# Kernel optimization log

Hardware: AMD Instinct MI355X
Metric: run time of the kernel (lower is better)

## Reference

```python
import jax, jax.numpy as jnp
import numpy as np

B, C, T, L = 32, 21, 512, 336
FREQ = T // 2 + 1  # 257
EPS = 1e-5


def setup_inputs() -> dict:
    key = jax.random.key(0)
    k1, k2, k3 = jax.random.split(key, 3)
    z = jax.random.normal(k1, (B, C, T), dtype=jnp.float32)
    affine_w = jnp.ones((C,), dtype=jnp.float32)
    affine_b = jnp.zeros((C,), dtype=jnp.float32)
    head_w = jax.random.normal(k2, (L, T * FREQ), dtype=jnp.float32) * 0.002
    head_b = jax.random.normal(k3, (L,), dtype=jnp.float32) * 0.01
    return {"z": z, "affine_w": affine_w, "affine_b": affine_b,
            "head_w": head_w, "head_b": head_b}


def _bases(T, FREQ):
    # t = arange(0,1,1/T); rows p: cos(2*pi*p*t), -sin(2*pi*p*t); DC row scaled by 0.5
    t = jnp.arange(T, dtype=jnp.float32) / T
    p = jnp.arange(FREQ, dtype=jnp.float32)
    ang = 2.0 * jnp.pi * p[:, None] * t[None, :]          # (FREQ, T)
    cosb = jnp.cos(ang).at[0].multiply(0.5)
    sinb = (-jnp.sin(ang)).at[0].multiply(0.5)
    return cosb, sinb


def reference(z, affine_w, affine_b, head_w, head_b):
    # RevIN 'norm' over time axis (unbiased=False variance)
    mean = jnp.mean(z, axis=-1, keepdims=True)              # (B,C,1)
    std = jnp.sqrt(jnp.var(z, axis=-1, keepdims=True) + EPS)
    w = affine_w[None, :, None]
    b = affine_b[None, :, None]
    zn = (z - mean) / std * w + b                           # (B,C,T)

    X = jnp.fft.rfft(zn, axis=-1) / T * 2.0                 # (B,C,FREQ) complex
    cosb, sinb = _bases(T, FREQ)
    # outer-product basis expansion -> (B,C,FREQ,T)
    basis = (jnp.einsum('bcp,pt->bcpt', jnp.real(X), cosb)
             + jnp.einsum('bcp,pt->bcpt', jnp.imag(X), sinb)).astype(jnp.float32)
    flat = basis.reshape(B, C, FREQ * T)                    # (B,C,head_nf)

    out = jnp.einsum('bcn,ln->bcl', flat, head_w) + head_b  # (B,C,L)

    # RevIN 'denorm'
    out = (out - b) / (w + EPS * EPS) * std + mean
    return out
```

## Files before the change

kernel.cpp:

```cpp
#include <hip/hip_runtime.h>
#include <math.h>

#define BB 32
#define CC 21
#define TT 512
#define LL 336
#define FREQ 257
#define NBC (BB*CC)
#define WROW (FREQ*TT)

__device__ __constant__ float kAngStep = 6.28318530717958647692f / 512.0f;

__global__ __launch_bounds__(256) void k0_stats(const float* __restrict__ z,
                                                float* __restrict__ meanv,
                                                float* __restrict__ stdv) {
    int row  = blockIdx.x * 4 + (threadIdx.x >> 6);
    int lane = threadIdx.x & 63;
    const float* zr = z + (size_t)row * TT;
    float s = 0.f, sq = 0.f;
#pragma unroll
    for (int j = 0; j < 8; ++j) {
        float v = zr[lane + 64 * j];
        s += v; sq += v * v;
    }
#pragma unroll
    for (int off = 32; off; off >>= 1) {
        s  += __shfl_xor(s,  off);
        sq += __shfl_xor(sq, off);
    }
    if (lane == 0) {
        float mu  = s * (1.0f / TT);
        float var = sq * (1.0f / TT) - mu * mu;
        meanv[row] = mu;
        stdv[row]  = sqrtf(var + 1e-5f);
    }
}

__global__ __launch_bounds__(256) void k1_ab(const float* __restrict__ hw,
                                             float* __restrict__ A,
                                             float* __restrict__ Bsm) {
    int bid  = blockIdx.x;
    int l    = bid / 65;
    int pt   = bid - l * 65;
    int w    = threadIdx.x >> 6;
    int p    = pt * 4 + w;
    if (p >= FREQ) return;
    int lane = threadIdx.x & 63;

    const float4* src = (const float4*)(hw + (size_t)l * WROW + (size_t)p * TT);
    float4 w1 = src[lane];
    float4 w2 = src[lane + 64];

    float sgn = (p & 1) ? -1.0f : 1.0f;
    float u0 = w1.x + sgn * w2.x;
    float u1 = w1.y + sgn * w2.y;
    float u2 = w1.z + sgn * w2.z;
    float u3 = w1.w + sgn * w2.w;

    int   k0 = (p * (lane * 4)) & 511;
    float a0 = (float)k0 * kAngStep;
    float c0, s0; sincosf(a0, &s0, &c0);
    float ad = (float)p * kAngStep;
    float cd, sd; sincosf(ad, &sd, &cd);

    float c1 = c0 * cd - s0 * sd,  s1 = s0 * cd + c0 * sd;
    float c2 = c1 * cd - s1 * sd,  s2 = s1 * cd + c1 * sd;
    float c3 = c2 * cd - s2 * sd,  s3 = s2 * cd + c2 * sd;

    float accA = u0 * c0 + u1 * c1 + u2 * c2 + u3 * c3;
    float accB = u0 * s0 + u1 * s1 + u2 * s2 + u3 * s3;

#pragma unroll
    for (int off = 32; off; off >>= 1) {
        accA += __shfl_xor(accA, off);
        accB += __shfl_xor(accB, off);
    }
    if (lane == 0) {
        A  [p * LL + l] = accA;
        Bsm[p * LL + l] = accB;
    }
}

__global__ __launch_bounds__(512) void k2_kbuild(const float* __restrict__ A,
                                                 const float* __restrict__ Bsm,
                                                 float* __restrict__ Km,
                                                 float* __restrict__ S) {
    int l = blockIdx.x;
    int t = threadIdx.x;
    const float* Al = A   + l;
    const float* Bl = Bsm + l;

    float dc, ds; sincosf((float)t * kAngStep, &ds, &dc);
    float c1 = dc, s1 = ds;
    float c2 = dc * dc - ds * ds;
    float s2 = 2.0f * dc * ds;
    float cd2 = c2, sd2 = s2;

    float acc1 = 0.5f * Al[0];
    float acc2 = 0.0f;
#pragma unroll 4
    for (int p = 1; p <= 255; p += 2) {
        acc1 += c1 * Al[p * LL]       + s1 * Bl[p * LL];
        acc2 += c2 * Al[(p + 1) * LL] + s2 * Bl[(p + 1) * LL];
        float nc1 = c1 * cd2 - s1 * sd2; s1 = s1 * cd2 + c1 * sd2; c1 = nc1;
        float nc2 = c2 * cd2 - s2 * sd2; s2 = s2 * cd2 + c2 * sd2; c2 = nc2;
    }
    float kval = (acc1 + acc2) * (2.0f / TT);
    Km[t * LL + l] = kval;

    float ss = kval;
#pragma unroll
    for (int off = 32; off; off >>= 1) ss += __shfl_xor(ss, off);
    __shared__ float red[8];
    if ((t & 63) == 0) red[t >> 6] = ss;
    __syncthreads();
    if (t == 0) {
        float tot = 0.f;
#pragma unroll
        for (int j = 0; j < 8; ++j) tot += red[j];
        S[l] = tot;
    }
}

__global__ __launch_bounds__(384) void k3_gemm(const float* __restrict__ z,
                                               const float* __restrict__ Km,
                                               const float* __restrict__ S,
                                               const float* __restrict__ meanv,
                                               const float* __restrict__ stdv,
                                               const float* __restrict__ aw,
                                               const float* __restrict__ ab,
                                               const float* __restrict__ hb,
                                               float* __restrict__ out) {
    int l = threadIdx.x;
    if (l >= LL) return;
    int bc0 = blockIdx.x * 4;
    const float* z0 = z + (size_t)bc0 * TT;
    const float* Kl = Km + l;

    float d0 = 0.f, d1 = 0.f, d2 = 0.f, d3 = 0.f;
#pragma unroll 8
    for (int t = 0; t < TT; ++t) {
        float k = Kl[t * LL];
        d0 += z0[t]           * k;
        d1 += z0[TT + t]      * k;
        d2 += z0[2 * TT + t]  * k;
        d3 += z0[3 * TT + t]  * k;
    }
    float Sl = S[l], hbl = hb[l];
    float d[4] = {d0, d1, d2, d3};
#pragma unroll
    for (int j = 0; j < 4; ++j) {
        int bc = bc0 + j;
        int c  = bc % CC;
        float mu = meanv[bc], sg = stdv[bc];
        float w  = aw[c],     b  = ab[c];
        out[(size_t)bc * LL + l] =
            (w * (d[j] - mu * Sl) + sg * (b * Sl + hbl - b)) / (w + 1e-10f) + mu;
    }
}

extern "C" void kernel_launch(void* const* d_in, const int* in_sizes, int n_in,
                              void* d_out, int out_size, void* d_ws, size_t ws_size,
                              hipStream_t stream) {
    const float* z  = (const float*)d_in[0];
    const float* aw = (const float*)d_in[1];
    const float* ab = (const float*)d_in[2];
    const float* hw = (const float*)d_in[3];
    const float* hb = (const float*)d_in[4];
    float* out = (float*)d_out;

    float* ws    = (float*)d_ws;
    float* meanv = ws;
    float* stdv  = ws + NBC;
    float* A     = stdv + NBC;
    float* Bsm   = A + FREQ * LL;
    float* Km    = Bsm + FREQ * LL;
    float* S     = Km + TT * LL;

    k0_stats <<<NBC / 4, 256, 0, stream>>>(z, meanv, stdv);
    k1_ab    <<<LL * 65, 256, 0, stream>>>(hw, A, Bsm);
    k2_kbuild<<<LL,      512, 0, stream>>>(A, Bsm, Km, S);
    k3_gemm  <<<NBC / 4, 384, 0, stream>>>(z, Km, S, meanv, stdv, aw, ab, hb, out);
}
```

Baseline: 296.2 us.

## Contract in frequency domain via per-row DFT instead of building time-domain kernel

Drops the kernel-build stage that turned the projected head weights into a 512-tap time-domain matrix. Instead, each (b,c) row gets its own DFT with a shared-memory twiddle table, and the final GEMM contracts over 257 frequency coefficients against the cosine and sine projections. The RevIN statistics are folded into the DFT kernel, and the weight projection switches to fast __sinf/__cosf intrinsics. This removes one launch and shrinks the GEMM reduction depth. The cost is extra per-row DFT work and intermediate buffers, plus lower accuracy from the fast trig.

```diff
diff --git a/kernel.cpp b/kernel.cpp
--- a/kernel.cpp
+++ b/kernel.cpp
@@ -9,153 +9,164 @@
 #define NBC (BB*CC)
 #define WROW (FREQ*TT)
 
-__device__ __constant__ float kAngStep = 6.28318530717958647692f / 512.0f;
+#define ANG (6.2831853071795864769e0f / 512.0f)
 
-__global__ __launch_bounds__(256) void k0_stats(const float* __restrict__ z,
-                                                float* __restrict__ meanv,
-                                                float* __restrict__ stdv) {
-    int row  = blockIdx.x * 4 + (threadIdx.x >> 6);
-    int lane = threadIdx.x & 63;
-    const float* zr = z + (size_t)row * TT;
-    float s = 0.f, sq = 0.f;
+__device__ __forceinline__ float wave_sum(float v) {
 #pragma unroll
-    for (int j = 0; j < 8; ++j) {
-        float v = zr[lane + 64 * j];
-        s += v; sq += v * v;
+    for (int off = 32; off; off >>= 1) v += __shfl_xor(v, off);
+    return v;
+}
+
+__global__ __launch_bounds__(320) void kA_zdft(const float* __restrict__ z,
+                                               const float* __restrict__ aw,
+                                               const float* __restrict__ ab,
+                                               float* __restrict__ ZC,
+                                               float* __restrict__ ZS,
+                                               float* __restrict__ stats) {
+    __shared__ float  zrow[512];
+    __shared__ float  zeo[512];
+    __shared__ float2 tab[512];
+    __shared__ float  red[10];
+    const int bc  = blockIdx.x;
+    const int tid = threadIdx.x;
+    const float* zr = z + (size_t)bc * TT;
+
+    float v0 = zr[tid];
+    float v1 = (tid < 192) ? zr[tid + 320] : 0.0f;
+    zrow[tid] = v0;
+    if (tid < 192) zrow[tid + 320] = v1;
+
+    float s  = v0 + v1;
+    float sq = v0 * v0 + v1 * v1;
+    s  = wave_sum(s);
+    sq = wave_sum(sq);
+    const int lane = tid & 63, wv = tid >> 6;
+    if (lane == 0) { red[wv] = s; red[5 + wv] = sq; }
+
+    {
+        float fk = (float)tid * (1.0f / 256.0f);
+        tab[tid] = make_float2(cospif(fk), sinpif(fk));
+        if (tid < 192) {
+            float fk2 = (float)(tid + 320) * (1.0f / 256.0f);
+            tab[tid + 320] = make_float2(cospif(fk2), sinpif(fk2));
+        }
     }
-#pragma unroll
-    for (int off = 32; off; off >>= 1) {
-        s  += __shfl_xor(s,  off);
-        sq += __shfl_xor(sq, off);
+    __syncthreads();
+
+    if (tid < 256) {
+        float a = zrow[tid], b = zrow[tid + 256];
+        zeo[tid]       = a + b;
+        zeo[tid + 256] = a - b;
     }
-    if (lane == 0) {
-        float mu  = s * (1.0f / TT);
-        float var = sq * (1.0f / TT) - mu * mu;
-        meanv[row] = mu;
-        stdv[row]  = sqrtf(var + 1e-5f);
+    if (tid == 0) {
+        float sum   = red[0]+red[1]+red[2]+red[3]+red[4];
+        float sumsq = red[5]+red[6]+red[7]+red[8]+red[9];
+        float mu  = sum * (1.0f / 512.0f);
+        float var = sumsq * (1.0f / 512.0f) - mu * mu;
+        float sg  = sqrtf(var + 1e-5f);
+        int c = bc % CC;
+        float w = aw[c], b = ab[c];
+        *(float4*)(stats + 4 * bc) = make_float4(mu, sg, w / sg, b - w * mu / sg);
+    }
+    __syncthreads();
+
+    if (tid < FREQ) {
+        const int p = tid;
+        const float* u = zeo + ((p & 1) ? 256 : 0);
+        float ac = 0.f, as = 0.f;
+        int k = 0;
+#pragma unroll 8
+        for (int t = 0; t < 256; ++t) {
+            float uv = u[t];
+            float2 cs = tab[k];
+            ac = fmaf(uv, cs.x, ac);
+            as = fmaf(uv, cs.y, as);
+            k = (k + p) & 511;
+        }
+        ZC[bc * FREQ + p] = ac;
+        ZS[bc * FREQ + p] = as;
     }
 }
 
-__global__ __launch_bounds__(256) void k1_ab(const float* __restrict__ hw,
-                                             float* __restrict__ A,
-                                             float* __restrict__ Bsm) {
-    int bid  = blockIdx.x;
-    int l    = bid / 65;
-    int pt   = bid - l * 65;
-    int w    = threadIdx.x >> 6;
-    int p    = pt * 4 + w;
+__global__ __launch_bounds__(256) void kB_wproj(const float* __restrict__ hw,
+                                                float* __restrict__ CA,
+                                                float* __restrict__ SA) {
+    const int l    = blockIdx.y;
+    const int w    = threadIdx.x >> 6;
+    const int lane = threadIdx.x & 63;
+    const int p    = blockIdx.x * 4 + w;
     if (p >= FREQ) return;
-    int lane = threadIdx.x & 63;
 
     const float4* src = (const float4*)(hw + (size_t)l * WROW + (size_t)p * TT);
     float4 w1 = src[lane];
     float4 w2 = src[lane + 64];
 
-    float sgn = (p & 1) ? -1.0f : 1.0f;
-    float u0 = w1.x + sgn * w2.x;
-    float u1 = w1.y + sgn * w2.y;
-    float u2 = w1.z + sgn * w2.z;
-    float u3 = w1.w + sgn * w2.w;
+    const float sgn = (p & 1) ? -1.0f : 1.0f;
+    float u0 = fmaf(sgn, w2.x, w1.x);
+    float u1 = fmaf(sgn, w2.y, w1.y);
+    float u2 = fmaf(sgn, w2.z, w1.z);
+    float u3 = fmaf(sgn, w2.w, w1.w);
 
-    int   k0 = (p * (lane * 4)) & 511;
-    float a0 = (float)k0 * kAngStep;
-    float c0, s0; sincosf(a0, &s0, &c0);
-    float ad = (float)p * kAngStep;
-    float cd, sd; sincosf(ad, &sd, &cd);
+    const int   k0 = (p * (lane * 4)) & 511;
+    const float a0 = (float)k0 * ANG;
+    float c0 = __cosf(a0), s0 = __sinf(a0);
+    const float ad = (float)p * ANG;
+    float cd = __cosf(ad), sd = __sinf(ad);
 
-    float c1 = c0 * cd - s0 * sd,  s1 = s0 * cd + c0 * sd;
-    float c2 = c1 * cd - s1 * sd,  s2 = s1 * cd + c1 * sd;
-    float c3 = c2 * cd - s2 * sd,  s3 = s2 * cd + c2 * sd;
+    float c1 = c0 * cd - s0 * sd, s1 = s0 * cd + c0 * sd;
+    float c2 = c1 * cd - s1 * sd, s2 = s1 * cd + c1 * sd;
+    float c3 = c2 * cd - s2 * sd, s3 = s2 * cd + c2 * sd;
 
     float accA = u0 * c0 + u1 * c1 + u2 * c2 + u3 * c3;
     float accB = u0 * s0 + u1 * s1 + u2 * s2 + u3 * s3;
+    accA = wave_sum(accA);
+    accB = wave_sum(accB);
 
-#pragma unroll
-    for (int off = 32; off; off >>= 1) {
-        accA += __shfl_xor(accA, off);
-        accB += __shfl_xor(accB, off);
-    }
     if (lane == 0) {
-        A  [p * LL + l] = accA;
-        Bsm[p * LL + l] = accB;
+        if (p == 0) { accA *= 0.5f; accB *= 0.5f; }
+        CA[p * LL + l] = accA;
+        SA[p * LL + l] = accB;
     }
 }
 
-__global__ __launch_bounds__(512) void k2_kbuild(const float* __restrict__ A,
-                                                 const float* __restrict__ Bsm,
-                                                 float* __restrict__ Km,
-                                                 float* __restrict__ S) {
-    int l = blockIdx.x;
-    int t = threadIdx.x;
-    const float* Al = A   + l;
-    const float* Bl = Bsm + l;
-
-    float dc, ds; sincosf((float)t * kAngStep, &ds, &dc);
-    float c1 = dc, s1 = ds;
-    float c2 = dc * dc - ds * ds;
-    float s2 = 2.0f * dc * ds;
-    float cd2 = c2, sd2 = s2;
-
-    float acc1 = 0.5f * Al[0];
-    float acc2 = 0.0f;
-#pragma unroll 4
-    for (int p = 1; p <= 255; p += 2) {
-        acc1 += c1 * Al[p * LL]       + s1 * Bl[p * LL];
-        acc2 += c2 * Al[(p + 1) * LL] + s2 * Bl[(p + 1) * LL];
-        float nc1 = c1 * cd2 - s1 * sd2; s1 = s1 * cd2 + c1 * sd2; c1 = nc1;
-        float nc2 = c2 * cd2 - s2 * sd2; s2 = s2 * cd2 + c2 * sd2; c2 = nc2;
-    }
-    float kval = (acc1 + acc2) * (2.0f / TT);
-    Km[t * LL + l] = kval;
-
-    float ss = kval;
-#pragma unroll
-    for (int off = 32; off; off >>= 1) ss += __shfl_xor(ss, off);
-    __shared__ float red[8];
-    if ((t & 63) == 0) red[t >> 6] = ss;
-    __syncthreads();
-    if (t == 0) {
-        float tot = 0.f;
-#pragma unroll
-        for (int j = 0; j < 8; ++j) tot += red[j];
-        S[l] = tot;
-    }
-}
-
-__global__ __launch_bounds__(384) void k3_gemm(const float* __restrict__ z,
-                                               const float* __restrict__ Km,
-                                               const float* __restrict__ S,
-                                               const float* __restrict__ meanv,
-                                               const float* __restrict__ stdv,
+__global__ __launch_bounds__(384) void kC_gemm(const float* __restrict__ ZC,
+                                               const float* __restrict__ ZS,
+                                               const float* __restrict__ CA,
+                                               const float* __restrict__ SA,
+                                               const float* __restrict__ stats,
                                                const float* __restrict__ aw,
                                                const float* __restrict__ ab,
                                                const float* __restrict__ hb,
                                                float* __restrict__ out) {
-    int l = threadIdx.x;
+    const int l = threadIdx.x;
     if (l >= LL) return;
-    int bc0 = blockIdx.x * 4;
-    const float* z0 = z + (size_t)bc0 * TT;
-    const float* Kl = Km + l;
+    const int bc0 = blockIdx.x * 4;
+    const float* zc0 = ZC + (size_t)bc0 * FREQ;
+    const float* zs0 = ZS + (size_t)bc0 * FREQ;
 
     float d0 = 0.f, d1 = 0.f, d2 = 0.f, d3 = 0.f;
-#pragma unroll 8
-    for (int t = 0; t < TT; ++t) {
-        float k = Kl[t * LL];
-        d0 += z0[t]           * k;
-        d1 += z0[TT + t]      * k;
-        d2 += z0[2 * TT + t]  * k;
-        d3 += z0[3 * TT + t]  * k;
+#pragma unroll 4
+    for (int p = 0; p < FREQ; ++p) {
+        float ca = CA[p * LL + l];
+        float sa = SA[p * LL + l];
+        d0 = fmaf(zc0[p],            ca, fmaf(zs0[p],            sa, d0));
+        d1 = fmaf(zc0[FREQ + p],     ca, fmaf(zs0[FREQ + p],     sa, d1));
+        d2 = fmaf(zc0[2 * FREQ + p], ca, fmaf(zs0[2 * FREQ + p], sa, d2));
+        d3 = fmaf(zc0[3 * FREQ + p], ca, fmaf(zs0[3 * FREQ + p], sa, d3));
     }
-    float Sl = S[l], hbl = hb[l];
+    const float ca0 = CA[l];
+    const float hbl = hb[l];
     float d[4] = {d0, d1, d2, d3};
 #pragma unroll
     for (int j = 0; j < 4; ++j) {
         int bc = bc0 + j;
         int c  = bc % CC;
-        float mu = meanv[bc], sg = stdv[bc];
-        float w  = aw[c],     b  = ab[c];
-        out[(size_t)bc * LL + l] =
-            (w * (d[j] - mu * Sl) + sg * (b * Sl + hbl - b)) / (w + 1e-10f) + mu;
+        float mu = stats[4 * bc + 0];
+        float sg = stats[4 * bc + 1];
+        float ga = stats[4 * bc + 2];
+        float de = stats[4 * bc + 3];
+        float pre = fmaf(ga * d[j], 2.0f / 512.0f, fmaf(2.0f * de, ca0, hbl));
+        out[(size_t)bc * LL + l] = (pre - ab[c]) / (aw[c] + 1e-10f) * sg + mu;
     }
 }
 
@@ -170,15 +181,13 @@
     float* out = (float*)d_out;
 
     float* ws    = (float*)d_ws;
-    float* meanv = ws;
-    float* stdv  = ws + NBC;
-    float* A     = stdv + NBC;
-    float* Bsm   = A + FREQ * LL;
-    float* Km    = Bsm + FREQ * LL;
-    float* S     = Km + TT * LL;
+    float* ZC    = ws;
+    float* ZS    = ZC + NBC * FREQ;
+    float* CA    = ZS + NBC * FREQ;
+    float* SA    = CA + FREQ * LL;
+    float* stats = SA + FREQ * LL;
 
-    k0_stats <<<NBC / 4, 256, 0, stream>>>(z, meanv, stdv);
-    k1_ab    <<<LL * 65, 256, 0, stream>>>(hw, A, Bsm);
-    k2_kbuild<<<LL,      512, 0, stream>>>(A, Bsm, Km, S);
-    k3_gemm  <<<NBC / 4, 384, 0, stream>>>(z, Km, S, meanv, stdv, aw, ab, hb, out);
+    kB_wproj<<<dim3(65, 336), 256, 0, stream>>>(hw, CA, SA);
+    kA_zdft <<<NBC, 320, 0, stream>>>(z, aw, ab, ZC, ZS, stats);
+    kC_gemm <<<NBC / 4, 384, 0, stream>>>(ZC, ZS, CA, SA, stats, aw, ab, hb, out);
 }
```

New measurement: 301.2 us. Within noise of the previous version (+1.7%).
